# Performance work log

Hardware: AMD Instinct MI355X
Metric: run time of the kernel (lower is better)

The kernel has to match this reference:

```python
import jax, jax.numpy as jnp
import numpy as np

N_CHUNKS = 2


def _sig_kernel(X, Y):
    """Signature kernel PDE solution K[:, -1, -1].
    X: (A, M, D), Y: (A, N, D). Effective grid is (M, N) (the original CUDA
    kernel's last row/col read OOB and are trimmed away).
    Recurrence: K[i,j] = K[i-1,j] + K[i,j-1] + K[i-1,j-1]*(inc[i-1,j-1]-1),
    K[0,:] = K[:,0] = 1.  For a fixed row i this is a cumulative sum:
    K[i,j] = 1 + cumsum_j( K[i-1,j] + K[i-1,j-1]*(inc-1) ).
    """
    dX = X[:, 1:] - X[:, :-1]                      # (A, M-1, D)
    dY = Y[:, 1:] - Y[:, :-1]                      # (A, N-1, D)
    inc = jnp.einsum('amd,and->amn', dX, dY)       # (A, M-1, N-1)
    n = inc.shape[2]
    dtype = inc.dtype

    def solve(inc_b):                              # inc_b: (M-1, N-1)
        row0 = jnp.ones(n + 1, dtype)

        def step(prev_row, inc_row):
            # c[j] = K[i-1,j+1] + K[i-1,j]*(inc[j]-1),  j = 0..n-1
            c = prev_row[1:] + prev_row[:-1] * (inc_row - 1.0)
            new_row = jnp.concatenate(
                [jnp.ones((1,), dtype), 1.0 + jnp.cumsum(c)])
            return new_row, None

        last_row, _ = jax.lax.scan(step, row0, inc_b)
        return last_row[-1]

    return jax.vmap(solve)(inc)                    # (A,)


def _sig_distance(x, y):
    return jnp.mean(_sig_kernel(x, x) + _sig_kernel(y, y)
                    - 2.0 * _sig_kernel(x, y))


def _sig_loss(X, Y, n_chunks=N_CHUNKS):
    if n_chunks == 1:
        return _sig_distance(X, Y)
    dist = jnp.zeros((), X.dtype)
    for k in range(2, n_chunks + 1):
        Xc = jnp.array_split(X, k, axis=1)
        Yc = jnp.array_split(Y, k, axis=1)
        for x1, x2, y1, y2 in zip(Xc[:-1], Xc[1:], Yc[:-1], Yc[1:]):
            dist = dist + _sig_distance(jnp.concatenate([x1, x2], axis=1),
                                        jnp.concatenate([y1, y2], axis=1))
    return dist


def setup_inputs() -> dict:
    key = jax.random.key(0)
    kx, ky = jax.random.split(key)
    A, L, D = 256, 256, 32
    SCALE = 0.02  # keep exp growth of the PDE solution in fp32 range
    X = SCALE * jax.random.normal(kx, (A, L, D), dtype=jnp.float32)
    Y = SCALE * jax.random.normal(ky, (A, L, D), dtype=jnp.float32)
    return {"X": X, "Y": Y}


def reference(X, Y):
    return _sig_loss(X, Y, n_chunks=N_CHUNKS)
```

## Files before the change

kernel.cpp:

```cpp
#include <hip/hip_runtime.h>


typedef _Float16 half8 __attribute__((ext_vector_type(8)));
typedef float f32x4_t __attribute__((ext_vector_type(4)));

#define DPP_ADD(v, ctrl, rmask)                                               \
    ((v) + __int_as_float(__builtin_amdgcn_update_dpp(                        \
               0, __float_as_int(v), (ctrl), (rmask), 0xF, true)))

#define INV2048 4.8828125e-4f

__global__ __launch_bounds__(64)
__attribute__((amdgpu_waves_per_eu(1, 1)))
void sig_pde(const float* __restrict__ X,
             const float* __restrict__ Y,
             float* __restrict__ partial) {
    const int bid = blockIdx.x;
    const int p = bid >> 8;
    const int a = bid & 255;
    const float* __restrict__ U = (p == 1) ? Y : X;
    const float* __restrict__ V = (p == 0) ? X : Y;
    U += (size_t)a * 256 * 32;
    V += (size_t)a * 256 * 32;
    const int lane = threadIdx.x;
    const int m16 = lane & 15;
    const int g2 = (lane >> 4) * 2;

    __shared__ __attribute__((aligned(16))) float incD[2][16 * 260];

    const float4* U4 = (const float4*)U;
    const float4* V4 = (const float4*)V;

    half8 bh[16], bl[16];
#pragma unroll
    for (int t = 0; t < 16; ++t) {
        int col = t * 16 + m16;
        int cp = (col + 1 < 256) ? col + 1 : 255;
        float4 lo0 = V4[col * 8 + g2], lo1 = V4[col * 8 + g2 + 1];
        float4 hi0 = V4[cp * 8 + g2],  hi1 = V4[cp * 8 + g2 + 1];
        float d[8] = {hi0.x - lo0.x, hi0.y - lo0.y, hi0.z - lo0.z, hi0.w - lo0.w,
                      hi1.x - lo1.x, hi1.y - lo1.y, hi1.z - lo1.z, hi1.w - lo1.w};
#pragma unroll
        for (int i = 0; i < 8; ++i) {
            _Float16 h = (_Float16)d[i];
            bh[t][i] = h;
            bl[t][i] = (_Float16)((d[i] - (float)h) * 2048.0f);
        }
    }

    float kp0 = 1.0f, kp1 = 1.0f, kp2 = 1.0f, kp3 = 1.0f;

    auto loadA = [&](int blk, float4 (&dst)[4]) {
        int r0 = blk * 16 + m16;
        int r1 = (r0 + 1 < 256) ? r0 + 1 : 255;
        dst[0] = U4[r0 * 8 + g2];
        dst[1] = U4[r0 * 8 + g2 + 1];
        dst[2] = U4[r1 * 8 + g2];
        dst[3] = U4[r1 * 8 + g2 + 1];
    };

    auto scan_row = [&](float4 mv) {
        float kn = __int_as_float(__builtin_amdgcn_update_dpp(
            0, __float_as_int(kp0), 0x130 , 0xF, 0xF, true));
        float c0 = fmaf(kp0, mv.x, kp1);
        float c1 = fmaf(kp1, mv.y, kp2);
        float c2 = fmaf(kp2, mv.z, kp3);
        float c3 = (lane == 63) ? 0.0f : fmaf(kp3, mv.w, kn);
        float L0 = c0, L1 = L0 + c1, L2 = L1 + c2;
        float T = L2 + c3;
        float S = T;
        S = DPP_ADD(S, 0x111, 0xF);
        S = DPP_ADD(S, 0x112, 0xF);
        S = DPP_ADD(S, 0x114, 0xF);
        S = DPP_ADD(S, 0x118, 0xF);
        S = DPP_ADD(S, 0x142, 0xA);
        S = DPP_ADD(S, 0x143, 0xC);
        float E = S - T;
        kp0 = 1.0f + E;
        kp1 = 1.0f + E + L0;
        kp2 = 1.0f + E + L1;
        kp3 = 1.0f + E + L2;
    };

#define RD(Gv, r) Gv = rp[(r) * 65 + lane]
    auto scan16 = [&](const float* buf, bool full) {
        const float4* rp = (const float4*)buf;
        float4 ga0, ga1, ga2, ga3, gb0, gb1, gb2, gb3;
        RD(ga0, 0); RD(ga1, 1); RD(ga2, 2); RD(ga3, 3);
        RD(gb0, 4); RD(gb1, 5); RD(gb2, 6); RD(gb3, 7);
        scan_row(ga0); scan_row(ga1); scan_row(ga2); scan_row(ga3);
        RD(ga0, 8); RD(ga1, 9); RD(ga2, 10); RD(ga3, 11);
        scan_row(gb0); scan_row(gb1); scan_row(gb2); scan_row(gb3);
        RD(gb0, 12); RD(gb1, 13); RD(gb2, 14);
        if (full) RD(gb3, 15);
        scan_row(ga0); scan_row(ga1); scan_row(ga2); scan_row(ga3);
        scan_row(gb0); scan_row(gb1); scan_row(gb2);
        if (full) scan_row(gb3);
    };
#undef RD

    auto mfma_block = [&](const float4 (&src)[4], float* __restrict__ buf) {
        float d[8] = {src[2].x - src[0].x, src[2].y - src[0].y,
                      src[2].z - src[0].z, src[2].w - src[0].w,
                      src[3].x - src[1].x, src[3].y - src[1].y,
                      src[3].z - src[1].z, src[3].w - src[1].w};
        half8 ah, al;
#pragma unroll
        for (int i = 0; i < 8; ++i) {
            _Float16 h = (_Float16)d[i];
            ah[i] = h;
            al[i] = (_Float16)((d[i] - (float)h) * 2048.0f);
        }
        const f32x4_t zero4 = {0.0f, 0.0f, 0.0f, 0.0f};
        const f32x4_t mone4 = {-1.0f, -1.0f, -1.0f, -1.0f};
        const int rb = (lane >> 4) << 2;
#pragma unroll
        for (int t = 0; t < 16; ++t) {
            f32x4_t acc2 =
                __builtin_amdgcn_mfma_f32_16x16x32_f16(ah, bl[t], zero4, 0, 0, 0);
            acc2 = __builtin_amdgcn_mfma_f32_16x16x32_f16(al, bh[t], acc2, 0, 0, 0);
            f32x4_t acc1 =
                __builtin_amdgcn_mfma_f32_16x16x32_f16(ah, bh[t], mone4, 0, 0, 0);
            int cc = t * 16 + m16;
            buf[(rb + 0) * 260 + cc] = fmaf(acc2[0], INV2048, acc1[0]);
            buf[(rb + 1) * 260 + cc] = fmaf(acc2[1], INV2048, acc1[1]);
            buf[(rb + 2) * 260 + cc] = fmaf(acc2[2], INV2048, acc1[2]);
            buf[(rb + 3) * 260 + cc] = fmaf(acc2[3], INV2048, acc1[3]);
        }
    };

    float4 A[4];
    loadA(0, A);
    mfma_block(A, incD[0]);
#pragma clang loop unroll(disable)
    for (int b = 1; b < 16; ++b) {
        loadA(b, A);
        scan16(incD[(b - 1) & 1], true);
        mfma_block(A, incD[b & 1]);
    }
    scan16(incD[1], false);

    if (lane == 63) {
        partial[bid] = (p == 2 ? -2.0f : 1.0f) * kp3;
    }
}

__global__ __launch_bounds__(256) void sig_reduce(const float* __restrict__ partial,
                                                  float* __restrict__ out) {
    const int t = threadIdx.x;
    float v = partial[t] + partial[t + 256] + partial[t + 512];
#pragma unroll
    for (int ofs = 32; ofs > 0; ofs >>= 1) v += __shfl_down(v, ofs);
    __shared__ float ws[4];
    if ((t & 63) == 0) ws[t >> 6] = v;
    __syncthreads();
    if (t == 0) out[0] = (ws[0] + ws[1] + ws[2] + ws[3]) * (1.0f / 256.0f);
}

extern "C" void kernel_launch(void* const* d_in, const int* in_sizes, int n_in,
                              void* d_out, int out_size, void* d_ws, size_t ws_size,
                              hipStream_t stream) {
    const float* X = (const float*)d_in[0];
    const float* Y = (const float*)d_in[1];
    float* partial = (float*)d_ws;
    sig_pde<<<dim3(768), dim3(64), 0, stream>>>(X, Y, partial);
    sig_reduce<<<dim3(1), dim3(256), 0, stream>>>(partial, (float*)d_out);
}
```

Before: 45.28 us.

## Interleave MFMA tiles with row scan and reformulate scan as affine in carry

The scan recurrence is rewritten so that each row's local partial sums are computed ahead of time as affine functions of the incoming carry E. Only one FMA then sits before the DPP prefix chain, which shortens the serial dependency per row. MFMA tile computation for the next block is interleaved with each scan row, and LDS reads are software-pipelined a few rows ahead. This hides MFMA and LDS latency behind the latency-bound scan, at the cost of more register pressure and a changed floating-point association order.

Result: slower. 46.63 us (+3.0%).

```diff
diff --git a/kernel.cpp b/kernel.cpp
--- a/kernel.cpp
+++ b/kernel.cpp
@@ -48,8 +48,6 @@
         }
     }
 
-    float kp0 = 1.0f, kp1 = 1.0f, kp2 = 1.0f, kp3 = 1.0f;
-
     auto loadA = [&](int blk, float4 (&dst)[4]) {
         int r0 = blk * 16 + m16;
         int r1 = (r0 + 1 < 256) ? r0 + 1 : 255;
@@ -58,90 +56,136 @@
         dst[2] = U4[r1 * 8 + g2];
         dst[3] = U4[r1 * 8 + g2 + 1];
     };
-
-    auto scan_row = [&](float4 mv) {
-        float kn = __int_as_float(__builtin_amdgcn_update_dpp(
-            0, __float_as_int(kp0), 0x130 , 0xF, 0xF, true));
-        float c0 = fmaf(kp0, mv.x, kp1);
-        float c1 = fmaf(kp1, mv.y, kp2);
-        float c2 = fmaf(kp2, mv.z, kp3);
-        float c3 = (lane == 63) ? 0.0f : fmaf(kp3, mv.w, kn);
-        float L0 = c0, L1 = L0 + c1, L2 = L1 + c2;
-        float T = L2 + c3;
-        float S = T;
-        S = DPP_ADD(S, 0x111, 0xF);
-        S = DPP_ADD(S, 0x112, 0xF);
-        S = DPP_ADD(S, 0x114, 0xF);
-        S = DPP_ADD(S, 0x118, 0xF);
-        S = DPP_ADD(S, 0x142, 0xA);
-        S = DPP_ADD(S, 0x143, 0xC);
-        float E = S - T;
-        kp0 = 1.0f + E;
-        kp1 = 1.0f + E + L0;
-        kp2 = 1.0f + E + L1;
-        kp3 = 1.0f + E + L2;
-    };
-
-#define RD(Gv, r) Gv = rp[(r) * 65 + lane]
-    auto scan16 = [&](const float* buf, bool full) {
-        const float4* rp = (const float4*)buf;
-        float4 ga0, ga1, ga2, ga3, gb0, gb1, gb2, gb3;
-        RD(ga0, 0); RD(ga1, 1); RD(ga2, 2); RD(ga3, 3);
-        RD(gb0, 4); RD(gb1, 5); RD(gb2, 6); RD(gb3, 7);
-        scan_row(ga0); scan_row(ga1); scan_row(ga2); scan_row(ga3);
-        RD(ga0, 8); RD(ga1, 9); RD(ga2, 10); RD(ga3, 11);
-        scan_row(gb0); scan_row(gb1); scan_row(gb2); scan_row(gb3);
-        RD(gb0, 12); RD(gb1, 13); RD(gb2, 14);
-        if (full) RD(gb3, 15);
-        scan_row(ga0); scan_row(ga1); scan_row(ga2); scan_row(ga3);
-        scan_row(gb0); scan_row(gb1); scan_row(gb2);
-        if (full) scan_row(gb3);
-    };
-#undef RD
-
-    auto mfma_block = [&](const float4 (&src)[4], float* __restrict__ buf) {
+    auto makeAhAl = [&](const float4 (&src)[4], half8& ah, half8& al) {
         float d[8] = {src[2].x - src[0].x, src[2].y - src[0].y,
                       src[2].z - src[0].z, src[2].w - src[0].w,
                       src[3].x - src[1].x, src[3].y - src[1].y,
                       src[3].z - src[1].z, src[3].w - src[1].w};
-        half8 ah, al;
 #pragma unroll
         for (int i = 0; i < 8; ++i) {
             _Float16 h = (_Float16)d[i];
             ah[i] = h;
             al[i] = (_Float16)((d[i] - (float)h) * 2048.0f);
         }
-        const f32x4_t zero4 = {0.0f, 0.0f, 0.0f, 0.0f};
-        const f32x4_t mone4 = {-1.0f, -1.0f, -1.0f, -1.0f};
-        const int rb = (lane >> 4) << 2;
-#pragma unroll
-        for (int t = 0; t < 16; ++t) {
-            f32x4_t acc2 =
-                __builtin_amdgcn_mfma_f32_16x16x32_f16(ah, bl[t], zero4, 0, 0, 0);
-            acc2 = __builtin_amdgcn_mfma_f32_16x16x32_f16(al, bh[t], acc2, 0, 0, 0);
-            f32x4_t acc1 =
-                __builtin_amdgcn_mfma_f32_16x16x32_f16(ah, bh[t], mone4, 0, 0, 0);
-            int cc = t * 16 + m16;
-            buf[(rb + 0) * 260 + cc] = fmaf(acc2[0], INV2048, acc1[0]);
-            buf[(rb + 1) * 260 + cc] = fmaf(acc2[1], INV2048, acc1[1]);
-            buf[(rb + 2) * 260 + cc] = fmaf(acc2[2], INV2048, acc1[2]);
-            buf[(rb + 3) * 260 + cc] = fmaf(acc2[3], INV2048, acc1[3]);
-        }
-    };
-
-    float4 A[4];
-    loadA(0, A);
-    mfma_block(A, incD[0]);
+    };
+
+    const f32x4_t zero4 = {0.0f, 0.0f, 0.0f, 0.0f};
+    const f32x4_t mone4 = {-1.0f, -1.0f, -1.0f, -1.0f};
+    const int rb = (lane >> 4) << 2;
+
+    auto tile = [&](int t, const half8& ah, const half8& al,
+                    float* __restrict__ buf) {
+        f32x4_t acc2 =
+            __builtin_amdgcn_mfma_f32_16x16x32_f16(ah, bl[t], zero4, 0, 0, 0);
+        acc2 = __builtin_amdgcn_mfma_f32_16x16x32_f16(al, bh[t], acc2, 0, 0, 0);
+        f32x4_t acc1 =
+            __builtin_amdgcn_mfma_f32_16x16x32_f16(ah, bh[t], mone4, 0, 0, 0);
+        int cc = t * 16 + m16;
+        buf[(rb + 0) * 260 + cc] = fmaf(acc2[0], INV2048, acc1[0]);
+        buf[(rb + 1) * 260 + cc] = fmaf(acc2[1], INV2048, acc1[1]);
+        buf[(rb + 2) * 260 + cc] = fmaf(acc2[2], INV2048, acc1[2]);
+        buf[(rb + 3) * 260 + cc] = fmaf(acc2[3], INV2048, acc1[3]);
+    };
+
+    float E = 0.0f;
+    float A_, Q_, aL0, aL1, aL2, qL0, qL1, qL2;
+    float lastL2 = 0.0f;
+
+    auto prep = [&](float4 m, float u1, float u2, float u3, float u4) {
+        float a0 = 1.0f + m.x, a1 = 1.0f + m.y;
+        float a2 = 1.0f + m.z, a3 = 1.0f + m.w;
+        float q0 = u1 + m.x;
+        float q1 = fmaf(u1, m.y, u2);
+        float q2 = fmaf(u2, m.z, u3);
+        float q3 = fmaf(u3, m.w, u4);
+        if (lane == 63) { a3 = 0.0f; q3 = 0.0f; }
+        aL0 = a0; aL1 = a0 + a1; aL2 = aL1 + a2; A_ = aL2 + a3;
+        qL0 = q0; qL1 = q0 + q1; qL2 = qL1 + q2; Q_ = qL2 + q3;
+    };
+
+    float4 Abuf[4];
+    loadA(0, Abuf);
+    half8 ah, al;
+    makeAhAl(Abuf, ah, al);
+#pragma unroll
+    for (int t = 0; t < 16; ++t) tile(t, ah, al, incD[0]);
+    loadA(1, Abuf);
+    {
+        const float4* rp0 = (const float4*)incD[0];
+        float4 m0 = rp0[0 * 65 + lane];
+        prep(m0, 1.0f, 1.0f, 1.0f, 1.0f);
+    }
+
 #pragma clang loop unroll(disable)
-    for (int b = 1; b < 16; ++b) {
-        loadA(b, A);
-        scan16(incD[(b - 1) & 1], true);
-        mfma_block(A, incD[b & 1]);
-    }
-    scan16(incD[1], false);
+    for (int pp = 1; pp < 16; ++pp) {
+        const float4* rp = (const float4*)incD[(pp - 1) & 1];
+        float* wb = incD[pp & 1];
+        makeAhAl(Abuf, ah, al);
+        if (pp + 1 < 16) loadA(pp + 1, Abuf);
+        float4 w[4];
+        w[0] = rp[1 * 65 + lane]; w[1] = rp[2 * 65 + lane];
+        w[2] = rp[3 * 65 + lane]; w[3] = rp[4 * 65 + lane];
+#pragma unroll
+        for (int k = 0; k < 16; ++k) {
+            tile(k, ah, al, wb);
+            float T = fmaf(E, A_, Q_);
+            float S = T;
+            S = DPP_ADD(S, 0x111, 0xF);
+            S = DPP_ADD(S, 0x112, 0xF);
+            S = DPP_ADD(S, 0x114, 0xF);
+            S = DPP_ADD(S, 0x118, 0xF);
+            S = DPP_ADD(S, 0x142, 0xA);
+            S = DPP_ADD(S, 0x143, 0xC);
+            float L0 = fmaf(E, aL0, qL0);
+            float L1 = fmaf(E, aL1, qL1);
+            float L2 = fmaf(E, aL2, qL2);
+            float u1 = 1.0f + L0, u2 = 1.0f + L1;
+            float u3 = 1.0f + L2, u4 = 1.0f + T;
+            float4 m;
+            if (k < 15) {
+                m = w[k & 3];
+                if (k <= 10) w[k & 3] = rp[(k + 5) * 65 + lane];
+            } else {
+                m = ((const float4*)wb)[0 * 65 + lane];
+            }
+            prep(m, u1, u2, u3, u4);
+            lastL2 = L2;
+            E = S - T;
+        }
+    }
+
+    {
+        const float4* rp = (const float4*)incD[1];
+        float4 w[4];
+        w[0] = rp[1 * 65 + lane]; w[1] = rp[2 * 65 + lane];
+        w[2] = rp[3 * 65 + lane]; w[3] = rp[4 * 65 + lane];
+#pragma unroll
+        for (int k = 0; k < 15; ++k) {
+            float T = fmaf(E, A_, Q_);
+            float S = T;
+            S = DPP_ADD(S, 0x111, 0xF);
+            S = DPP_ADD(S, 0x112, 0xF);
+            S = DPP_ADD(S, 0x114, 0xF);
+            S = DPP_ADD(S, 0x118, 0xF);
+            S = DPP_ADD(S, 0x142, 0xA);
+            S = DPP_ADD(S, 0x143, 0xC);
+            float L0 = fmaf(E, aL0, qL0);
+            float L1 = fmaf(E, aL1, qL1);
+            float L2 = fmaf(E, aL2, qL2);
+            if (k < 14) {
+                float u1 = 1.0f + L0, u2 = 1.0f + L1;
+                float u3 = 1.0f + L2, u4 = 1.0f + T;
+                float4 m = w[k & 3];
+                if (k <= 9) w[k & 3] = rp[(k + 5) * 65 + lane];
+                prep(m, u1, u2, u3, u4);
+            }
+            lastL2 = L2;
+            E = S - T;
+        }
+    }
 
     if (lane == 63) {
-        partial[bid] = (p == 2 ? -2.0f : 1.0f) * kp3;
+        partial[bid] = (p == 2 ? -2.0f : 1.0f) * (1.0f + E + lastL2);
     }
 }
 
```

## Interleave MFMA tile computation with row scans in a software-pipelined loop

Applied to the files above, without the earlier changes.

The separate scan16 and mfma_block phases are merged into one loop that issues the three MFMAs for one column tile, then runs one row scan, so matrix-core latency can hide behind the DPP-based scan work. Shared-memory reads for the scan now use a 4-deep rotating register prefetch. The two low-part MFMAs are made independent (each accumulates from zero, then the results are added) to shorten the dependency chain. This adds a vector add per tile and raises register pressure and instruction-scheduling complexity in exchange for overlapping the two phases.

New measurement: 47.73 us. 1.05x slower.

```diff
diff --git a/kernel.cpp b/kernel.cpp
--- a/kernel.cpp
+++ b/kernel.cpp
@@ -58,6 +58,18 @@
         dst[2] = U4[r1 * 8 + g2];
         dst[3] = U4[r1 * 8 + g2 + 1];
     };
+    auto makeAhAl = [&](const float4 (&src)[4], half8& ah, half8& al) {
+        float d[8] = {src[2].x - src[0].x, src[2].y - src[0].y,
+                      src[2].z - src[0].z, src[2].w - src[0].w,
+                      src[3].x - src[1].x, src[3].y - src[1].y,
+                      src[3].z - src[1].z, src[3].w - src[1].w};
+#pragma unroll
+        for (int i = 0; i < 8; ++i) {
+            _Float16 h = (_Float16)d[i];
+            ah[i] = h;
+            al[i] = (_Float16)((d[i] - (float)h) * 2048.0f);
+        }
+    };
 
     auto scan_row = [&](float4 mv) {
         float kn = __int_as_float(__builtin_amdgcn_update_dpp(
@@ -82,63 +94,72 @@
         kp3 = 1.0f + E + L2;
     };
 
-#define RD(Gv, r) Gv = rp[(r) * 65 + lane]
-    auto scan16 = [&](const float* buf, bool full) {
-        const float4* rp = (const float4*)buf;
-        float4 ga0, ga1, ga2, ga3, gb0, gb1, gb2, gb3;
-        RD(ga0, 0); RD(ga1, 1); RD(ga2, 2); RD(ga3, 3);
-        RD(gb0, 4); RD(gb1, 5); RD(gb2, 6); RD(gb3, 7);
-        scan_row(ga0); scan_row(ga1); scan_row(ga2); scan_row(ga3);
-        RD(ga0, 8); RD(ga1, 9); RD(ga2, 10); RD(ga3, 11);
-        scan_row(gb0); scan_row(gb1); scan_row(gb2); scan_row(gb3);
-        RD(gb0, 12); RD(gb1, 13); RD(gb2, 14);
-        if (full) RD(gb3, 15);
-        scan_row(ga0); scan_row(ga1); scan_row(ga2); scan_row(ga3);
-        scan_row(gb0); scan_row(gb1); scan_row(gb2);
-        if (full) scan_row(gb3);
-    };
-#undef RD
-
-    auto mfma_block = [&](const float4 (&src)[4], float* __restrict__ buf) {
-        float d[8] = {src[2].x - src[0].x, src[2].y - src[0].y,
-                      src[2].z - src[0].z, src[2].w - src[0].w,
-                      src[3].x - src[1].x, src[3].y - src[1].y,
-                      src[3].z - src[1].z, src[3].w - src[1].w};
-        half8 ah, al;
-#pragma unroll
-        for (int i = 0; i < 8; ++i) {
-            _Float16 h = (_Float16)d[i];
-            ah[i] = h;
-            al[i] = (_Float16)((d[i] - (float)h) * 2048.0f);
-        }
-        const f32x4_t zero4 = {0.0f, 0.0f, 0.0f, 0.0f};
-        const f32x4_t mone4 = {-1.0f, -1.0f, -1.0f, -1.0f};
-        const int rb = (lane >> 4) << 2;
-#pragma unroll
-        for (int t = 0; t < 16; ++t) {
-            f32x4_t acc2 =
-                __builtin_amdgcn_mfma_f32_16x16x32_f16(ah, bl[t], zero4, 0, 0, 0);
-            acc2 = __builtin_amdgcn_mfma_f32_16x16x32_f16(al, bh[t], acc2, 0, 0, 0);
-            f32x4_t acc1 =
-                __builtin_amdgcn_mfma_f32_16x16x32_f16(ah, bh[t], mone4, 0, 0, 0);
-            int cc = t * 16 + m16;
-            buf[(rb + 0) * 260 + cc] = fmaf(acc2[0], INV2048, acc1[0]);
-            buf[(rb + 1) * 260 + cc] = fmaf(acc2[1], INV2048, acc1[1]);
-            buf[(rb + 2) * 260 + cc] = fmaf(acc2[2], INV2048, acc1[2]);
-            buf[(rb + 3) * 260 + cc] = fmaf(acc2[3], INV2048, acc1[3]);
-        }
-    };
+    const f32x4_t zero4 = {0.0f, 0.0f, 0.0f, 0.0f};
+    const f32x4_t mone4 = {-1.0f, -1.0f, -1.0f, -1.0f};
+    const int rb = (lane >> 4) << 2;
 
     float4 A[4];
     loadA(0, A);
-    mfma_block(A, incD[0]);
+    half8 ah, al;
+    makeAhAl(A, ah, al);
+    {
+        float* __restrict__ wb = incD[0];
+#pragma unroll
+        for (int t = 0; t < 16; ++t) {
+            f32x4_t a2a = __builtin_amdgcn_mfma_f32_16x16x32_f16(
+                ah, bl[t], zero4, 0, 0, 0);
+            f32x4_t a2b = __builtin_amdgcn_mfma_f32_16x16x32_f16(
+                al, bh[t], zero4, 0, 0, 0);
+            f32x4_t a1 = __builtin_amdgcn_mfma_f32_16x16x32_f16(
+                ah, bh[t], mone4, 0, 0, 0);
+            f32x4_t s = a2a + a2b;
+            int cc = t * 16 + m16;
+            wb[(rb + 0) * 260 + cc] = fmaf(s[0], INV2048, a1[0]);
+            wb[(rb + 1) * 260 + cc] = fmaf(s[1], INV2048, a1[1]);
+            wb[(rb + 2) * 260 + cc] = fmaf(s[2], INV2048, a1[2]);
+            wb[(rb + 3) * 260 + cc] = fmaf(s[3], INV2048, a1[3]);
+        }
+    }
+
 #pragma clang loop unroll(disable)
     for (int b = 1; b < 16; ++b) {
         loadA(b, A);
-        scan16(incD[(b - 1) & 1], true);
-        mfma_block(A, incD[b & 1]);
+        const float4* rp = (const float4*)incD[(b - 1) & 1];
+        float* __restrict__ wb = incD[b & 1];
+        makeAhAl(A, ah, al);
+        float4 w[4];
+        w[0] = rp[0 * 65 + lane]; w[1] = rp[1 * 65 + lane];
+        w[2] = rp[2 * 65 + lane]; w[3] = rp[3 * 65 + lane];
+#pragma unroll
+        for (int k = 0; k < 16; ++k) {
+            f32x4_t a2a = __builtin_amdgcn_mfma_f32_16x16x32_f16(
+                ah, bl[k], zero4, 0, 0, 0);
+            f32x4_t a2b = __builtin_amdgcn_mfma_f32_16x16x32_f16(
+                al, bh[k], zero4, 0, 0, 0);
+            f32x4_t a1 = __builtin_amdgcn_mfma_f32_16x16x32_f16(
+                ah, bh[k], mone4, 0, 0, 0);
+            scan_row(w[k & 3]);
+            if (k + 4 < 16) w[k & 3] = rp[(k + 4) * 65 + lane];
+            f32x4_t s = a2a + a2b;
+            int cc = k * 16 + m16;
+            wb[(rb + 0) * 260 + cc] = fmaf(s[0], INV2048, a1[0]);
+            wb[(rb + 1) * 260 + cc] = fmaf(s[1], INV2048, a1[1]);
+            wb[(rb + 2) * 260 + cc] = fmaf(s[2], INV2048, a1[2]);
+            wb[(rb + 3) * 260 + cc] = fmaf(s[3], INV2048, a1[3]);
+        }
     }
-    scan16(incD[1], false);
+
+    {
+        const float4* rp = (const float4*)incD[1];
+        float4 w[4];
+        w[0] = rp[0 * 65 + lane]; w[1] = rp[1 * 65 + lane];
+        w[2] = rp[2 * 65 + lane]; w[3] = rp[3 * 65 + lane];
+#pragma unroll
+        for (int k = 0; k < 15; ++k) {
+            scan_row(w[k & 3]);
+            if (k + 4 < 15) w[k & 3] = rp[(k + 4) * 65 + lane];
+        }
+    }
 
     if (lane == 63) {
         partial[bid] = (p == 2 ? -2.0f : 1.0f) * kp3;
```
